# Performance work log

Hardware: AMD Instinct MI355X
Metric: run time of the kernel (lower is better)

Reference implementation:

```python
import jax, jax.numpy as jnp
import numpy as np

B, S, D, F = 8, 2048, 1024, 3072
EPS = 1e-6


def _rmsnorm(x, w):
    rms = jax.lax.rsqrt(jnp.mean(x * x, axis=-1, keepdims=True) + EPS)
    return x * rms * w


def _scan_causal(x_scan, a):
    # h_t = a_t * h_{t-1} + x_t, over time axis. x_scan, a: [B,S,D]
    def step(h, inp):
        xs, at = inp
        h = at * h + xs
        return h, h
    xs_t = jnp.swapaxes(x_scan, 0, 1)  # [S,B,D]
    a_t = jnp.swapaxes(a, 0, 1)
    h0 = jnp.zeros(x_scan.shape[::2], dtype=x_scan.dtype)  # [B,D]
    _, out = jax.lax.scan(step, h0, (xs_t, a_t))
    return jnp.swapaxes(out, 0, 1)  # [B,S,D]


def setup_inputs() -> dict:
    key = jax.random.key(0)
    ks = jax.random.split(key, 12)
    sd = 1.0 / np.sqrt(D)
    sf = 1.0 / np.sqrt(F)
    return {
        "x": jax.random.normal(ks[0], (B, S, D), dtype=jnp.float32),
        "rms_mix_w": jnp.ones((D,), jnp.float32),
        "rms_ffn_w": jnp.ones((D,), jnp.float32),
        "Wg": jax.random.uniform(ks[1], (D, D), jnp.float32, -sd, sd),
        "bg": jax.random.uniform(ks[2], (D,), jnp.float32, -sd, sd),
        "Wv": jax.random.uniform(ks[3], (D, D), jnp.float32, -sd, sd),
        "bv": jax.random.uniform(ks[4], (D,), jnp.float32, -sd, sd),
        "Wd": jax.random.uniform(ks[5], (D, D), jnp.float32, -sd, sd),
        "bd": jnp.full((D,), 1.0, jnp.float32),  # decay_bias_init = 1.0
        "W_gate": jax.random.uniform(ks[6], (F, D), jnp.float32, -sd, sd),
        "W_up": jax.random.uniform(ks[7], (F, D), jnp.float32, -sd, sd),
        "W_out": jax.random.uniform(ks[8], (D, F), jnp.float32, -sf, sf),
    }


def reference(x, rms_mix_w, rms_ffn_w, Wg, bg, Wv, bv, Wd, bd, W_gate, W_up, W_out):
    # --- MinGRU mixer with pre-RMSNorm and residual ---
    xn = _rmsnorm(x, rms_mix_w)
    g = jnp.einsum("bsd,ed->bse", xn, Wg) + bg
    v = jnp.einsum("bsd,ed->bse", xn, Wv) + bv
    d = jnp.einsum("bsd,ed->bse", xn, Wd) + bd
    x_scan = jax.nn.sigmoid(g) * jnp.tanh(v)
    a = 0.001 + 0.998 * jax.nn.sigmoid(d)
    x = x + _scan_causal(x_scan, a)
    # --- SwiGLU FFN with pre-RMSNorm and residual ---
    xn = _rmsnorm(x, rms_ffn_w)
    gate = jax.nn.silu(jnp.einsum("bsd,fd->bsf", xn, W_gate))
    up = jnp.einsum("bsd,fd->bsf", xn, W_up)
    x = x + jnp.einsum("bsf,df->bsd", gate * up, W_out)
    return x
```

## Files before the change

kernel.cpp:

```cpp
#include <hip/hip_runtime.h>
#include <cstdint>
#include <cstddef>

typedef unsigned short u16;
typedef __attribute__((ext_vector_type(4))) float f32x4;
typedef __attribute__((ext_vector_type(8))) short s16x8;

#define BB 8
#define SS 2048
#define DD 1024
#define FF 3072
#define MM (BB*SS)
#define NCH 64
#define LCH (SS/NCH)

__device__ __forceinline__ float bf2f(u16 u){ union{uint32_t i;float f;}v; v.i=((uint32_t)u)<<16; return v.f; }
__device__ __forceinline__ u16 f2bf(float f){ union{float f;uint32_t i;}v; v.f=f; uint32_t r=v.i+0x7FFFu+((v.i>>16)&1u); return (u16)(r>>16); }
__device__ __forceinline__ float sigm(float x){ return 1.f/(1.f+__expf(-x)); }
__device__ __forceinline__ float tanh_f(float x){ return 2.f*sigm(2.f*x)-1.f; }

__global__ void conv_all(const float* __restrict__ Wg, const float* __restrict__ Wv,
                         const float* __restrict__ Wd, const float* __restrict__ Wgate,
                         const float* __restrict__ Wup, const float* __restrict__ Wout,
                         const float* __restrict__ rfw,
                         u16* __restrict__ oGvd, u16* __restrict__ oGu, u16* __restrict__ oWo){
  const int blk = blockIdx.x;
  if (blk < 3072) {
    size_t i = ((size_t)blk*256 + threadIdx.x)*4;
    int row = (int)(i >> 10); int col = (int)(i & 1023);
    const float* src; int srow;
    if (row < 2048) { int grp = row >> 5, w = row & 31; src = (w < 16) ? Wg : Wv; srow = grp*16 + (w & 15); }
    else            { src = Wd; srow = row - 2048; }
    float4 v = *(const float4*)(src + (size_t)srow*1024 + col);
    ushort4 o; o.x=f2bf(v.x); o.y=f2bf(v.y); o.z=f2bf(v.z); o.w=f2bf(v.w);
    *(ushort4*)(oGvd + i) = o;
  } else if (blk < 9216) {
    size_t i = ((size_t)(blk-3072)*256 + threadIdx.x)*4;
    int row = (int)(i >> 10); int col = (int)(i & 1023);
    int group = row >> 5, w = row & 31;
    const float* src = (w < 16) ? Wgate : Wup;
    int srow = group*16 + (w & 15);
    float4 v = *(const float4*)(src + (size_t)srow*1024 + col);
    float4 s = *(const float4*)(rfw + col);
    ushort4 o; o.x=f2bf(v.x*s.x); o.y=f2bf(v.y*s.y); o.z=f2bf(v.z*s.z); o.w=f2bf(v.w*s.w);
    *(ushort4*)(oGu + i) = o;
  } else {
    size_t i = ((size_t)(blk-9216)*256 + threadIdx.x)*4;
    float4 v = *(const float4*)(Wout + i);
    ushort4 o; o.x=f2bf(v.x); o.y=f2bf(v.y); o.z=f2bf(v.z); o.w=f2bf(v.w);
    *(ushort4*)(oWo + i) = o;
  }
}

__global__ void rmsnorm_k(const float* __restrict__ x, const float* __restrict__ wgt,
                          u16* __restrict__ out){
  const int row = blockIdx.x, t = threadIdx.x;
  float4 v = ((const float4*)(x + (size_t)row*DD))[t];
  float ss = v.x*v.x + v.y*v.y + v.z*v.z + v.w*v.w;
  #pragma unroll
  for (int o = 32; o > 0; o >>= 1) ss += __shfl_down(ss, o, 64);
  __shared__ float sacc[4];
  if ((t & 63) == 0) sacc[t >> 6] = ss;
  __syncthreads();
  float tot = sacc[0] + sacc[1] + sacc[2] + sacc[3];
  float r = rsqrtf(tot * (1.f/(float)DD) + 1e-6f);
  float4 wv = ((const float4*)wgt)[t];
  ushort4 o; o.x=f2bf(v.x*r*wv.x); o.y=f2bf(v.y*r*wv.y); o.z=f2bf(v.z*r*wv.z); o.w=f2bf(v.w*r*wv.w);
  ((ushort4*)(out + (size_t)row*DD))[t] = o;
}

template<int EPI, int NTN>
__global__ __launch_bounds__(512) void gemm256(
    const u16* __restrict__ A, const u16* __restrict__ Bm, int K,
    const float* __restrict__ bg, const float* __restrict__ bv, const float* __restrict__ bd,
    const float* __restrict__ rinv,
    u16* __restrict__ o_xs, u16* __restrict__ o_a,
    u16* __restrict__ o_h, const u16* __restrict__ yres, float* __restrict__ o_out)
{
  __shared__ u16 lds[2*32768];
  const int tid = threadIdx.x, w = tid >> 6, l = tid & 63;
  const int wr = w >> 2, wc = w & 3;
  const int nwg = gridDim.x, bid = blockIdx.x;
  const int sw = (bid & 7) * (nwg >> 3) + (bid >> 3);
  const int tm = sw / NTN, tn = sw % NTN;

  const int srow  = w*8 + (l >> 3);
  const int sslot = (l & 7) ^ ((l >> 3) & 7);
  const u16* gA = A  + (size_t)(tm*256 + srow)*K + sslot*8;
  const u16* gB = Bm + (size_t)(tn*256 + srow)*K + sslot*8;

#define STAGE_HALF(dbuf, isB, h, tile) do { \
    const u16* gsrc_ = ((isB) ? gB : gA) + ((size_t)(h)*128)*K + (size_t)(tile)*64; \
    u16* ldst_ = &lds[(dbuf)*32768 + (isB)*16384 + (h)*8192 + w*512]; \
    __builtin_amdgcn_global_load_lds((const __attribute__((address_space(1))) void*)gsrc_, \
        (__attribute__((address_space(3))) void*)ldst_, 16, 0, 0); \
    __builtin_amdgcn_global_load_lds((const __attribute__((address_space(1))) void*)(gsrc_ + (size_t)64*K), \
        (__attribute__((address_space(3))) void*)(ldst_ + 4096), 16, 0, 0); \
  } while(0)

  const int aRow = wr*128 + (l & 15);
  const int bRow = wc*64  + (l & 15);
  const int sl0  = (((l >> 4) ^ (l & 7))) * 8;

#define LDA(cb, mi, ks) (*(const s16x8*)&lds[(cb)*32768 + (aRow + (mi)*16)*64 + (sl0 ^ ((ks)*32))])
#define LDB(cb, ni, ks) (*(const s16x8*)&lds[(cb)*32768 + 16384 + (bRow + (ni)*16)*64 + (sl0 ^ ((ks)*32))])

#define LOADB(cb) do { \
    bfr[0][0]=LDB(cb,0,0); bfr[0][1]=LDB(cb,0,1); \
    bfr[1][0]=LDB(cb,1,0); bfr[1][1]=LDB(cb,1,1); \
    bfr[2][0]=LDB(cb,2,0); bfr[2][1]=LDB(cb,2,1); \
    bfr[3][0]=LDB(cb,3,0); bfr[3][1]=LDB(cb,3,1); \
  } while(0)

#define PHASE(cb, mi0, STAGE_STMT, ...) do { \
    s16x8 a00 = LDA(cb, (mi0),   0), a01 = LDA(cb, (mi0),   1); \
    s16x8 a10 = LDA(cb, (mi0)+1, 0), a11 = LDA(cb, (mi0)+1, 1); \
    STAGE_STMT; \
    asm volatile("s_waitcnt lgkmcnt(0)" ::: "memory"); \
    __VA_ARGS__; \
    __builtin_amdgcn_s_barrier(); \
    __builtin_amdgcn_s_setprio(1); \
    acc[(mi0)  ][0] = __builtin_amdgcn_mfma_f32_16x16x32_bf16(a00, bfr[0][0], acc[(mi0)  ][0],0,0,0); \
    acc[(mi0)  ][1] = __builtin_amdgcn_mfma_f32_16x16x32_bf16(a00, bfr[1][0], acc[(mi0)  ][1],0,0,0); \
    acc[(mi0)  ][2] = __builtin_amdgcn_mfma_f32_16x16x32_bf16(a00, bfr[2][0], acc[(mi0)  ][2],0,0,0); \
    acc[(mi0)  ][3] = __builtin_amdgcn_mfma_f32_16x16x32_bf16(a00, bfr[3][0], acc[(mi0)  ][3],0,0,0); \
    acc[(mi0)+1][0] = __builtin_amdgcn_mfma_f32_16x16x32_bf16(a10, bfr[0][0], acc[(mi0)+1][0],0,0,0); \
    acc[(mi0)+1][1] = __builtin_amdgcn_mfma_f32_16x16x32_bf16(a10, bfr[1][0], acc[(mi0)+1][1],0,0,0); \
    acc[(mi0)+1][2] = __builtin_amdgcn_mfma_f32_16x16x32_bf16(a10, bfr[2][0], acc[(mi0)+1][2],0,0,0); \
    acc[(mi0)+1][3] = __builtin_amdgcn_mfma_f32_16x16x32_bf16(a10, bfr[3][0], acc[(mi0)+1][3],0,0,0); \
    acc[(mi0)  ][0] = __builtin_amdgcn_mfma_f32_16x16x32_bf16(a01, bfr[0][1], acc[(mi0)  ][0],0,0,0); \
    acc[(mi0)  ][1] = __builtin_amdgcn_mfma_f32_16x16x32_bf16(a01, bfr[1][1], acc[(mi0)  ][1],0,0,0); \
    acc[(mi0)  ][2] = __builtin_amdgcn_mfma_f32_16x16x32_bf16(a01, bfr[2][1], acc[(mi0)  ][2],0,0,0); \
    acc[(mi0)  ][3] = __builtin_amdgcn_mfma_f32_16x16x32_bf16(a01, bfr[3][1], acc[(mi0)  ][3],0,0,0); \
    acc[(mi0)+1][0] = __builtin_amdgcn_mfma_f32_16x16x32_bf16(a11, bfr[0][1], acc[(mi0)+1][0],0,0,0); \
    acc[(mi0)+1][1] = __builtin_amdgcn_mfma_f32_16x16x32_bf16(a11, bfr[1][1], acc[(mi0)+1][1],0,0,0); \
    acc[(mi0)+1][2] = __builtin_amdgcn_mfma_f32_16x16x32_bf16(a11, bfr[2][1], acc[(mi0)+1][2],0,0,0); \
    acc[(mi0)+1][3] = __builtin_amdgcn_mfma_f32_16x16x32_bf16(a11, bfr[3][1], acc[(mi0)+1][3],0,0,0); \
    __builtin_amdgcn_s_setprio(0); \
  } while(0)

  f32x4 acc[8][4] = {};
  s16x8 bfr[4][2];
  const int nk = K >> 6;

  STAGE_HALF(0,0,0,0); STAGE_HALF(0,0,1,0);
  STAGE_HALF(0,1,0,0); STAGE_HALF(0,1,1,0);
  STAGE_HALF(1,1,0,1); STAGE_HALF(1,1,1,1);
  asm volatile("s_waitcnt vmcnt(4)" ::: "memory");
  __builtin_amdgcn_s_barrier();

  for (int it = 0, t = 0; it < (nk >> 1); ++it, t += 2) {
    const int tp1 = t + 1;
    int tp2 = t + 2; if (tp2 >= nk) tp2 -= nk;
    int tp3 = t + 3; if (tp3 >= nk) tp3 -= nk;
    LOADB(0);
    PHASE(0, 0, STAGE_HALF(1,0,0,tp1), );
    PHASE(0, 2, STAGE_HALF(1,0,1,tp1), );
    PHASE(0, 4, STAGE_HALF(0,1,0,tp2), );
    PHASE(0, 6, STAGE_HALF(0,1,1,tp2), asm volatile("s_waitcnt vmcnt(4)" ::: "memory"));
    LOADB(1);
    PHASE(1, 0, STAGE_HALF(0,0,0,tp2), );
    PHASE(1, 2, STAGE_HALF(0,0,1,tp2), );
    PHASE(1, 4, STAGE_HALF(1,1,0,tp3), );
    PHASE(1, 6, STAGE_HALF(1,1,1,tp3), asm volatile("s_waitcnt vmcnt(4)" ::: "memory"));
  }
#undef PHASE
#undef LOADB
#undef LDA
#undef LDB
#undef STAGE_HALF

  const int rb = tm*256 + wr*128 + ((l >> 4) << 2);
  const int lc = l & 15;
  if constexpr (EPI == 0) {
    if (tn < 8) {
      #pragma unroll
      for (int mi = 0; mi < 8; ++mi)
        #pragma unroll
        for (int j = 0; j < 2; ++j) {
          int f = tn*128 + wc*32 + j*16 + lc;
          float bgf = bg[f], bvf = bv[f];
          #pragma unroll
          for (int i = 0; i < 4; ++i) {
            int r = rb + mi*16 + i;
            float g2 = acc[mi][2*j][i]   + bgf;
            float v2 = acc[mi][2*j+1][i] + bvf;
            o_xs[(size_t)r*DD + f] = f2bf(sigm(g2) * tanh_f(v2));
          }
        }
    } else {
      #pragma unroll
      for (int mi = 0; mi < 8; ++mi)
        #pragma unroll
        for (int ni = 0; ni < 4; ++ni) {
          int c = (tn-8)*256 + wc*64 + ni*16 + lc;
          float bdc = bd[c];
          #pragma unroll
          for (int i = 0; i < 4; ++i) {
            int r = rb + mi*16 + i;
            o_a[(size_t)r*DD + c] = f2bf(0.001f + 0.998f*sigm(acc[mi][ni][i] + bdc));
          }
        }
    }
  } else if constexpr (EPI == 1) {
    #pragma unroll
    for (int mi = 0; mi < 8; ++mi) {
      float4 rv = *(const float4*)&rinv[rb + mi*16];
      #pragma unroll
      for (int j = 0; j < 2; ++j) {
        int f = tn*128 + wc*32 + j*16 + lc;
        #pragma unroll
        for (int i = 0; i < 4; ++i) {
          int r = rb + mi*16 + i;
          float rvi = (i==0) ? rv.x : (i==1) ? rv.y : (i==2) ? rv.z : rv.w;
          float g2 = acc[mi][2*j][i]*rvi, u2 = acc[mi][2*j+1][i]*rvi;
          o_h[(size_t)r*FF + f] = f2bf(g2 * sigm(g2) * u2);
        }
      }
    }
  } else {
    #pragma unroll
    for (int mi = 0; mi < 8; ++mi)
      #pragma unroll
      for (int ni = 0; ni < 4; ++ni) {
        int c = tn*256 + wc*64 + ni*16 + lc;
        #pragma unroll
        for (int i = 0; i < 4; ++i) {
          int r = rb + mi*16 + i;
          size_t idx = (size_t)r*DD + c;
          o_out[idx] = bf2f(yres[idx]) + acc[mi][ni][i];
        }
      }
  }
}

__global__ void scan_pass1(const u16* __restrict__ xs, const u16* __restrict__ ab,
                           float* __restrict__ Ac, float* __restrict__ Xc){
  const int bid = blockIdx.x;
  const int d = ((bid & 3) << 8) + threadIdx.x;
  const int c = (bid >> 2) & (NCH-1);
  const int b = bid >> 8;
  size_t base = ((size_t)b*SS + (size_t)c*LCH)*DD + d;
  float A = 1.f, X = 0.f;
  for (int tt = 0; tt < LCH; ++tt){
    size_t idx = base + (size_t)tt*DD;
    float a = bf2f(ab[idx]);
    X = a*X + bf2f(xs[idx]); A *= a;
  }
  size_t o = ((size_t)b*NCH + c)*DD + d;
  Ac[o] = A; Xc[o] = X;
}

__global__ void scan_pass2(const float* __restrict__ Ac, const float* __restrict__ Xc,
                           float* __restrict__ hin){
  int gid = blockIdx.x*256 + threadIdx.x;
  int b = gid >> 10, d = gid & 1023;
  float h = 0.f;
  for (int c = 0; c < NCH; ++c){
    size_t o = ((size_t)b*NCH + c)*DD + d;
    hin[o] = h;
    h = Ac[o]*h + Xc[o];
  }
}

__global__ __launch_bounds__(256) void scan_pass3_y(
    const u16* __restrict__ xs, const u16* __restrict__ ab,
    const float* __restrict__ hin, const float* __restrict__ x,
    u16* __restrict__ ybf, float* __restrict__ rinv)
{
  const int bid = blockIdx.x;
  const int c = bid & (NCH-1);
  const int b = bid >> 6;
  const int t = threadIdx.x;
  float h[4];
  size_t hb = ((size_t)b*NCH + c)*DD + t;
  #pragma unroll
  for (int j = 0; j < 4; ++j) h[j] = hin[hb + j*256];
  __shared__ float sred[4];
  size_t base = ((size_t)b*SS + (size_t)c*LCH)*DD + t;
  const int row0 = b*SS + c*LCH;
  for (int tt = 0; tt < LCH; ++tt){
    size_t rowb = base + (size_t)tt*DD;
    float yv[4]; float ss = 0.f;
    #pragma unroll
    for (int j = 0; j < 4; ++j){
      size_t idx = rowb + (size_t)j*256;
      float a = bf2f(ab[idx]);
      h[j] = a*h[j] + bf2f(xs[idx]);
      yv[j] = x[idx] + h[j];
      ss += yv[j]*yv[j];
    }
    #pragma unroll
    for (int o = 32; o > 0; o >>= 1) ss += __shfl_down(ss, o, 64);
    if ((t & 63) == 0) sred[t >> 6] = ss;
    __syncthreads();
    float tot = sred[0] + sred[1] + sred[2] + sred[3];
    float r = rsqrtf(tot * (1.f/(float)DD) + 1e-6f);
    if (t == 0) rinv[row0 + tt] = r;
    #pragma unroll
    for (int j = 0; j < 4; ++j){
      size_t idx = rowb + (size_t)j*256;
      ybf[idx] = f2bf(yv[j]);
    }
    __syncthreads();
  }
}

extern "C" void kernel_launch(void* const* d_in, const int* in_sizes, int n_in,
                              void* d_out, int out_size, void* d_ws, size_t ws_size,
                              hipStream_t stream) {
  const float* x     = (const float*)d_in[0];
  const float* rmw   = (const float*)d_in[1];
  const float* rfw   = (const float*)d_in[2];
  const float* Wg    = (const float*)d_in[3];
  const float* bg    = (const float*)d_in[4];
  const float* Wv    = (const float*)d_in[5];
  const float* bv    = (const float*)d_in[6];
  const float* Wd    = (const float*)d_in[7];
  const float* bd    = (const float*)d_in[8];
  const float* Wgate = (const float*)d_in[9];
  const float* Wup   = (const float*)d_in[10];
  const float* Wout  = (const float*)d_in[11];
  float* out = (float*)d_out;

  char* p = (char*)d_ws;
  u16*  xn    = (u16*)p;              p += (size_t)MM*DD*2;
  u16*  Wgvd  = (u16*)p;              p += (size_t)3072*1024*2;
  u16*  Wgu   = (u16*)p;              p += (size_t)6144*1024*2;
  u16*  Wo    = (u16*)p;              p += (size_t)1024*3072*2;
  char* big   = p;                    p += (size_t)MM*FF*2;
  u16*  xs    = (u16*)big;
  u16*  ab    = (u16*)(big + (size_t)MM*DD*2);
  u16*  hbuf  = (u16*)big;
  float* Ac   = (float*)p;            p += (size_t)BB*NCH*DD*4;
  float* Xc   = (float*)p;            p += (size_t)BB*NCH*DD*4;
  float* hin  = (float*)p;            p += (size_t)BB*NCH*DD*4;
  float* rinv = (float*)p;            p += (size_t)MM*4;
  u16*  ybf   = xn;

  conv_all<<<12288, 256, 0, stream>>>(Wg, Wv, Wd, Wgate, Wup, Wout, rfw, Wgvd, Wgu, Wo);

  rmsnorm_k<<<MM, 256, 0, stream>>>(x, rmw, xn);
  gemm256<0,12><<<64*12, 512, 0, stream>>>(xn, Wgvd, 1024,
      bg, bv, bd, nullptr, xs, ab, nullptr, nullptr, nullptr);
  scan_pass1<<<BB*NCH*4, 256, 0, stream>>>(xs, ab, Ac, Xc);
  scan_pass2<<<32, 256, 0, stream>>>(Ac, Xc, hin);
  scan_pass3_y<<<BB*NCH, 256, 0, stream>>>(xs, ab, hin, x, ybf, rinv);

  gemm256<1,24><<<64*24, 512, 0, stream>>>(ybf, Wgu, 1024,
      nullptr, nullptr, nullptr, rinv, nullptr, nullptr, hbuf, nullptr, nullptr);
  gemm256<2,4><<<64*4, 512, 0, stream>>>(hbuf, Wo, 3072,
      nullptr, nullptr, nullptr, nullptr, nullptr, nullptr, nullptr, ybf, out);
}
```

Before: 501.4 us.

## Software-pipeline LDS fragment loads one phase ahead of MFMA in GEMM loop

Restructures the GEMM main loop so the A fragments for the next phase (and B fragments for the next buffer) are loaded from LDS right after the barrier, while the current phase's MFMAs run on registers loaded in the previous phase. The explicit lgkmcnt(0) wait before each barrier is removed, so LDS reads overlap with matrix math instead of stalling. Uses double-buffered register sets (two A sets, two B sets), which raises VGPR pressure and depends on the compiler inserting correct waits for the LDS reads.

```diff
diff --git a/kernel.cpp b/kernel.cpp
--- a/kernel.cpp
+++ b/kernel.cpp
@@ -105,42 +105,48 @@
 #define LDA(cb, mi, ks) (*(const s16x8*)&lds[(cb)*32768 + (aRow + (mi)*16)*64 + (sl0 ^ ((ks)*32))])
 #define LDB(cb, ni, ks) (*(const s16x8*)&lds[(cb)*32768 + 16384 + (bRow + (ni)*16)*64 + (sl0 ^ ((ks)*32))])
 
-#define LOADB(cb) do { \
-    bfr[0][0]=LDB(cb,0,0); bfr[0][1]=LDB(cb,0,1); \
-    bfr[1][0]=LDB(cb,1,0); bfr[1][1]=LDB(cb,1,1); \
-    bfr[2][0]=LDB(cb,2,0); bfr[2][1]=LDB(cb,2,1); \
-    bfr[3][0]=LDB(cb,3,0); bfr[3][1]=LDB(cb,3,1); \
+#define LDA4(P, cb, mi0) do { \
+    P##0 = LDA(cb, (mi0),   0); P##1 = LDA(cb, (mi0),   1); \
+    P##2 = LDA(cb, (mi0)+1, 0); P##3 = LDA(cb, (mi0)+1, 1); \
   } while(0)
 
-#define PHASE(cb, mi0, STAGE_STMT, ...) do { \
-    s16x8 a00 = LDA(cb, (mi0),   0), a01 = LDA(cb, (mi0),   1); \
-    s16x8 a10 = LDA(cb, (mi0)+1, 0), a11 = LDA(cb, (mi0)+1, 1); \
-    STAGE_STMT; \
-    asm volatile("s_waitcnt lgkmcnt(0)" ::: "memory"); \
+#define LDB8(P, cb) do { \
+    P##_00=LDB(cb,0,0); P##_01=LDB(cb,0,1); \
+    P##_10=LDB(cb,1,0); P##_11=LDB(cb,1,1); \
+    P##_20=LDB(cb,2,0); P##_21=LDB(cb,2,1); \
+    P##_30=LDB(cb,3,0); P##_31=LDB(cb,3,1); \
+  } while(0)
+
+#define VMW4 asm volatile("s_waitcnt vmcnt(4)" ::: "memory")
+
+#define PH(STG, VMW, MI0, A0,A1,A2,A3, B00,B01,B10,B11,B20,B21,B30,B31, ...) do { \
+    STG; VMW; \
+    __builtin_amdgcn_s_barrier(); \
     __VA_ARGS__; \
-    __builtin_amdgcn_s_barrier(); \
     __builtin_amdgcn_s_setprio(1); \
-    acc[(mi0)  ][0] = __builtin_amdgcn_mfma_f32_16x16x32_bf16(a00, bfr[0][0], acc[(mi0)  ][0],0,0,0); \
-    acc[(mi0)  ][1] = __builtin_amdgcn_mfma_f32_16x16x32_bf16(a00, bfr[1][0], acc[(mi0)  ][1],0,0,0); \
-    acc[(mi0)  ][2] = __builtin_amdgcn_mfma_f32_16x16x32_bf16(a00, bfr[2][0], acc[(mi0)  ][2],0,0,0); \
-    acc[(mi0)  ][3] = __builtin_amdgcn_mfma_f32_16x16x32_bf16(a00, bfr[3][0], acc[(mi0)  ][3],0,0,0); \
-    acc[(mi0)+1][0] = __builtin_amdgcn_mfma_f32_16x16x32_bf16(a10, bfr[0][0], acc[(mi0)+1][0],0,0,0); \
-    acc[(mi0)+1][1] = __builtin_amdgcn_mfma_f32_16x16x32_bf16(a10, bfr[1][0], acc[(mi0)+1][1],0,0,0); \
-    acc[(mi0)+1][2] = __builtin_amdgcn_mfma_f32_16x16x32_bf16(a10, bfr[2][0], acc[(mi0)+1][2],0,0,0); \
-    acc[(mi0)+1][3] = __builtin_amdgcn_mfma_f32_16x16x32_bf16(a10, bfr[3][0], acc[(mi0)+1][3],0,0,0); \
-    acc[(mi0)  ][0] = __builtin_amdgcn_mfma_f32_16x16x32_bf16(a01, bfr[0][1], acc[(mi0)  ][0],0,0,0); \
-    acc[(mi0)  ][1] = __builtin_amdgcn_mfma_f32_16x16x32_bf16(a01, bfr[1][1], acc[(mi0)  ][1],0,0,0); \
-    acc[(mi0)  ][2] = __builtin_amdgcn_mfma_f32_16x16x32_bf16(a01, bfr[2][1], acc[(mi0)  ][2],0,0,0); \
-    acc[(mi0)  ][3] = __builtin_amdgcn_mfma_f32_16x16x32_bf16(a01, bfr[3][1], acc[(mi0)  ][3],0,0,0); \
-    acc[(mi0)+1][0] = __builtin_amdgcn_mfma_f32_16x16x32_bf16(a11, bfr[0][1], acc[(mi0)+1][0],0,0,0); \
-    acc[(mi0)+1][1] = __builtin_amdgcn_mfma_f32_16x16x32_bf16(a11, bfr[1][1], acc[(mi0)+1][1],0,0,0); \
-    acc[(mi0)+1][2] = __builtin_amdgcn_mfma_f32_16x16x32_bf16(a11, bfr[2][1], acc[(mi0)+1][2],0,0,0); \
-    acc[(mi0)+1][3] = __builtin_amdgcn_mfma_f32_16x16x32_bf16(a11, bfr[3][1], acc[(mi0)+1][3],0,0,0); \
+    acc[(MI0)  ][0] = __builtin_amdgcn_mfma_f32_16x16x32_bf16(A0, B00, acc[(MI0)  ][0],0,0,0); \
+    acc[(MI0)  ][1] = __builtin_amdgcn_mfma_f32_16x16x32_bf16(A0, B10, acc[(MI0)  ][1],0,0,0); \
+    acc[(MI0)  ][2] = __builtin_amdgcn_mfma_f32_16x16x32_bf16(A0, B20, acc[(MI0)  ][2],0,0,0); \
+    acc[(MI0)  ][3] = __builtin_amdgcn_mfma_f32_16x16x32_bf16(A0, B30, acc[(MI0)  ][3],0,0,0); \
+    acc[(MI0)+1][0] = __builtin_amdgcn_mfma_f32_16x16x32_bf16(A2, B00, acc[(MI0)+1][0],0,0,0); \
+    acc[(MI0)+1][1] = __builtin_amdgcn_mfma_f32_16x16x32_bf16(A2, B10, acc[(MI0)+1][1],0,0,0); \
+    acc[(MI0)+1][2] = __builtin_amdgcn_mfma_f32_16x16x32_bf16(A2, B20, acc[(MI0)+1][2],0,0,0); \
+    acc[(MI0)+1][3] = __builtin_amdgcn_mfma_f32_16x16x32_bf16(A2, B30, acc[(MI0)+1][3],0,0,0); \
+    acc[(MI0)  ][0] = __builtin_amdgcn_mfma_f32_16x16x32_bf16(A1, B01, acc[(MI0)  ][0],0,0,0); \
+    acc[(MI0)  ][1] = __builtin_amdgcn_mfma_f32_16x16x32_bf16(A1, B11, acc[(MI0)  ][1],0,0,0); \
+    acc[(MI0)  ][2] = __builtin_amdgcn_mfma_f32_16x16x32_bf16(A1, B21, acc[(MI0)  ][2],0,0,0); \
+    acc[(MI0)  ][3] = __builtin_amdgcn_mfma_f32_16x16x32_bf16(A1, B31, acc[(MI0)  ][3],0,0,0); \
+    acc[(MI0)+1][0] = __builtin_amdgcn_mfma_f32_16x16x32_bf16(A3, B01, acc[(MI0)+1][0],0,0,0); \
+    acc[(MI0)+1][1] = __builtin_amdgcn_mfma_f32_16x16x32_bf16(A3, B11, acc[(MI0)+1][1],0,0,0); \
+    acc[(MI0)+1][2] = __builtin_amdgcn_mfma_f32_16x16x32_bf16(A3, B21, acc[(MI0)+1][2],0,0,0); \
+    acc[(MI0)+1][3] = __builtin_amdgcn_mfma_f32_16x16x32_bf16(A3, B31, acc[(MI0)+1][3],0,0,0); \
     __builtin_amdgcn_s_setprio(0); \
   } while(0)
 
   f32x4 acc[8][4] = {};
-  s16x8 bfr[4][2];
+  s16x8 aX0,aX1,aX2,aX3, aY0,aY1,aY2,aY3;
+  s16x8 b0_00,b0_01,b0_10,b0_11,b0_20,b0_21,b0_30,b0_31;
+  s16x8 b1_00,b1_01,b1_10,b1_11,b1_20,b1_21,b1_30,b1_31;
   const int nk = K >> 6;
 
   STAGE_HALF(0,0,0,0); STAGE_HALF(0,0,1,0);
@@ -148,24 +154,34 @@
   STAGE_HALF(1,1,0,1); STAGE_HALF(1,1,1,1);
   asm volatile("s_waitcnt vmcnt(4)" ::: "memory");
   __builtin_amdgcn_s_barrier();
+  LDB8(b0, 0);
+  LDA4(aX, 0, 0);
 
   for (int it = 0, t = 0; it < (nk >> 1); ++it, t += 2) {
     const int tp1 = t + 1;
     int tp2 = t + 2; if (tp2 >= nk) tp2 -= nk;
     int tp3 = t + 3; if (tp3 >= nk) tp3 -= nk;
-    LOADB(0);
-    PHASE(0, 0, STAGE_HALF(1,0,0,tp1), );
-    PHASE(0, 2, STAGE_HALF(1,0,1,tp1), );
-    PHASE(0, 4, STAGE_HALF(0,1,0,tp2), );
-    PHASE(0, 6, STAGE_HALF(0,1,1,tp2), asm volatile("s_waitcnt vmcnt(4)" ::: "memory"));
-    LOADB(1);
-    PHASE(1, 0, STAGE_HALF(0,0,0,tp2), );
-    PHASE(1, 2, STAGE_HALF(0,0,1,tp2), );
-    PHASE(1, 4, STAGE_HALF(1,1,0,tp3), );
-    PHASE(1, 6, STAGE_HALF(1,1,1,tp3), asm volatile("s_waitcnt vmcnt(4)" ::: "memory"));
-  }
-#undef PHASE
-#undef LOADB
+    PH(STAGE_HALF(1,0,0,tp1),     , 0, aX0,aX1,aX2,aX3, b0_00,b0_01,b0_10,b0_11,b0_20,b0_21,b0_30,b0_31,
+       LDA4(aY,0,2));
+    PH(STAGE_HALF(1,0,1,tp1),     , 2, aY0,aY1,aY2,aY3, b0_00,b0_01,b0_10,b0_11,b0_20,b0_21,b0_30,b0_31,
+       LDA4(aX,0,4));
+    PH(STAGE_HALF(0,1,0,tp2),     , 4, aX0,aX1,aX2,aX3, b0_00,b0_01,b0_10,b0_11,b0_20,b0_21,b0_30,b0_31,
+       LDA4(aY,0,6));
+    PH(STAGE_HALF(0,1,1,tp2), VMW4, 6, aY0,aY1,aY2,aY3, b0_00,b0_01,b0_10,b0_11,b0_20,b0_21,b0_30,b0_31,
+       LDA4(aX,1,0); LDB8(b1,1));
+    PH(STAGE_HALF(0,0,0,tp2),     , 0, aX0,aX1,aX2,aX3, b1_00,b1_01,b1_10,b1_11,b1_20,b1_21,b1_30,b1_31,
+       LDA4(aY,1,2));
+    PH(STAGE_HALF(0,0,1,tp2),     , 2, aY0,aY1,aY2,aY3, b1_00,b1_01,b1_10,b1_11,b1_20,b1_21,b1_30,b1_31,
+       LDA4(aX,1,4));
+    PH(STAGE_HALF(1,1,0,tp3),     , 4, aX0,aX1,aX2,aX3, b1_00,b1_01,b1_10,b1_11,b1_20,b1_21,b1_30,b1_31,
+       LDA4(aY,1,6));
+    PH(STAGE_HALF(1,1,1,tp3), VMW4, 6, aY0,aY1,aY2,aY3, b1_00,b1_01,b1_10,b1_11,b1_20,b1_21,b1_30,b1_31,
+       LDA4(aX,0,0); LDB8(b0,0));
+  }
+#undef PH
+#undef VMW4
+#undef LDA4
+#undef LDB8
 #undef LDA
 #undef LDB
 #undef STAGE_HALF
```

New measurement: 1.044 ms. +108.1%, slower.
